# Optimization experiments

Hardware: AMD Instinct MI355X
Metric: run time of the kernel (lower is better)

## Reference

```python
import jax, jax.numpy as jnp
import numpy as np
from jax.scipy.special import logsumexp

B, L, M, D = 8192, 1024, 128, 2  # batch, hilbert.size, bond dim, local_size
MACHINE_POW = 2


def setup_inputs() -> dict:
    key = jax.random.key(0)
    k1, k2 = jax.random.split(key)
    # configurations in the zero-magnetization sector: each row is a permutation
    # of L//2 zeros and L//2 ones (constrained HomogeneousHilbert)
    base = jnp.tile(jnp.arange(D, dtype=jnp.int32), L // D)  # (L,)
    inputs = jax.vmap(lambda k: jax.random.permutation(k, base))(jax.random.split(k1, B))
    # variational parameters epsilon: (local_size, M, size); centered at 1 so the
    # length-L multiplicative cache chain stays in fp32 range
    epsilon = 1.0 + 0.02 * jax.random.normal(k2, (D, M, L), dtype=jnp.float32)
    return {"inputs": inputs, "epsilon": epsilon}


def _conditionals(inputs, epsilon):
    # inputs: (B, L) int in [0, D); epsilon: (D, M, L)
    Bn, Ln = inputs.shape
    Dn, Mn, _ = epsilon.shape
    half = Ln // 2

    def scan_fun(carry, index):
        cache, n_spins = carry                       # (B, D, M), (B, D)
        prev = inputs[:, (index - 1) % Ln]           # (B,) previous-site state
        params_i = epsilon[:, :, index]              # (D, M)
        # irregular gather: cache[b, prev[b], :]
        gathered = jnp.take_along_axis(cache, prev[:, None, None], axis=1)[:, 0, :]  # (B, M)
        prods = params_i[None, :, :] * gathered[:, None, :]  # (B, D, M)
        log_psi = jnp.sum(prods, axis=-1)            # (B, D) sum over bond dim
        n_spins = jnp.where(index > 0,
                            n_spins + jax.nn.one_hot(prev, Dn, dtype=jnp.int32),
                            n_spins)
        # zero-magnetization renormalization: -inf once a local state is exhausted
        renorm = jnp.log(jnp.heaviside((half - n_spins).astype(log_psi.dtype), 0.0))
        return (prods, n_spins), log_psi + renorm

    cache0 = jnp.ones((Bn, Dn, Mn), epsilon.dtype)
    n0 = jnp.zeros((Bn, Dn), jnp.int32)
    _, log_psi = jax.lax.scan(scan_fun, (cache0, n0), jnp.arange(Ln))
    return jnp.transpose(log_psi, (1, 0, 2))  # (B, L, D)


def reference(inputs, epsilon):
    lp = _conditionals(inputs, epsilon)  # (B, L, D)
    # normalize conditionals over local states (machine_pow = 2)
    lp = lp - (1.0 / MACHINE_POW) * logsumexp(MACHINE_POW * lp, axis=-1, keepdims=True)
    # pick the log-conditional of the actual configuration at each site
    sel = jnp.take_along_axis(lp, inputs[:, :, None], axis=2)[:, :, 0]  # (B, L)
    # n_symm = 1 (default apply_symmetries): symmetrized logsumexp is identity
    return jnp.sum(sel, axis=1)  # (B,) log_psi
```

## Files before the change

### kernel.cpp

```cpp
#include <hip/hip_runtime.h>
#include <hip/hip_fp16.h>

typedef unsigned long long u64;
typedef unsigned int uint32;
typedef short short8 __attribute__((ext_vector_type(8)));
typedef float f32x4 __attribute__((ext_vector_type(4)));
typedef _Float16 h2 __attribute__((ext_vector_type(2)));

#define B_N 8192
#define L_N 1024
#define M_N 128
#define C_N 16
#define CH_N 64
#define HALF_N 512

#define OFF_W16  0
#define OFF_R16  0x40000
#define OFF_BITS 0x80000
#define OFF_LR   0x180000
#define OFF_RQ   0x1C0000
#define OFF_T    0x21C0000

#define PACK_BLK 2048
#define PACK_IT  16
#define EPS_BLK  32
#define ZERO_BLK 32

__device__ __forceinline__ unsigned short f32_bf16(float f) {
    union { float f; unsigned u; } x; x.f = f;
    unsigned u = x.u + 0x7FFFu + ((x.u >> 16) & 1u);
    return (unsigned short)(u >> 16);
}

__device__ __forceinline__ float fdot2(h2 a, h2 b, float c) {
#if __has_builtin(__builtin_amdgcn_fdot2)
    return __builtin_amdgcn_fdot2(a, b, c, false);
#else
    return (float)a[0] * (float)b[0] + (float)a[1] * (float)b[1] + c;
#endif
}

__device__ __forceinline__ uint32 fas_u(float f) { union { float f; uint32 u; } x; x.f = f; return x.u; }
__device__ __forceinline__ float uas_f(uint32 u) { union { uint32 u; float f; } x; x.u = u; return x.f; }

template<int CTRL>
__device__ __forceinline__ float dpp_add(float x, float y) {
    union { float f; int i; } a, r;
    a.f = y;
    r.i = __builtin_amdgcn_update_dpp(0, a.i, CTRL, 0xF, 0xF, true);
    return x + r.f;
}

union HU { uint32 u; __half2 hh; h2 v2; };

__global__ __launch_bounds__(256) void k_prep(const int* __restrict__ inp,
        const float* __restrict__ eps, u64* __restrict__ bits,
        _Float16* __restrict__ w16, _Float16* __restrict__ r16,
        unsigned short* __restrict__ lrT, float* __restrict__ out) {
    int bid = blockIdx.x;
    if (bid < PACK_BLK) {
        int g = bid * 256 + threadIdx.x;
        const int stride = PACK_BLK * 256;
        #pragma unroll 4
        for (int it = 0; it < PACK_IT; ++it) {
            int v = inp[g];
            u64 m = __ballot(v != 0);
            if ((threadIdx.x & 63) == 0) bits[g >> 6] = m;
            g += stride;
        }
        return;
    }
    bid -= PACK_BLK;
    if (bid < EPS_BLK) {
        int wid = threadIdx.x >> 6, lane = threadIdx.x & 63;
        int m = bid * 4 + wid;
        const float* e0 = eps + (size_t)m * L_N + lane * 16;
        const float* e1 = eps + (size_t)(M_N + m) * L_N + lane * 16;
        float a[16], b[16];
        #pragma unroll
        for (int j = 0; j < 16; j += 4) {
            *(float4*)&a[j] = *(const float4*)&e0[j];
            *(float4*)&b[j] = *(const float4*)&e1[j];
        }
        float local = 1.f;
        #pragma unroll
        for (int j = 0; j < 16; ++j) local *= a[j];
        float sc = local;
        #pragma unroll
        for (int d = 1; d < 64; d <<= 1) {
            float up = __shfl_up(sc, d);
            if (lane >= d) sc *= up;
        }
        float prev = __shfl_up(sc, 1);
        float E = (lane == 0) ? 1.f : prev;
        int i0 = lane * 16;
        #pragma unroll
        for (int j = 0; j < 16; ++j) {
            float rat = b[j] / a[j];
            w16[(size_t)(i0 + j) * M_N + m] = (_Float16)(E * (a[j] - b[j]));
            r16[(size_t)(i0 + j) * M_N + m] = (_Float16)(rat - 1.f);
            lrT[(size_t)m * L_N + i0 + j] = f32_bf16(__log2f(rat));
            E *= a[j];
        }
        return;
    }
    bid -= EPS_BLK;
    if (bid < ZERO_BLK) {
        out[bid * 256 + threadIdx.x] = 0.f;
    }
}

__global__ __launch_bounds__(256) void k_slog2(const u64* __restrict__ bits,
        const unsigned short* __restrict__ lrT, _Float16* __restrict__ Rq,
        int* __restrict__ T) {
    if (blockIdx.x >= 1024) {
        int b = (blockIdx.x - 1024) * 256 + threadIdx.x;
        const u64* brow = bits + (size_t)b * 16;
        int n1 = 0, n0 = 0, Tv = 1024;
        for (int wd = 0; wd < 16; ++wd) {
            u64 x = brow[wd];
            int pc = __popcll(x);
            if (n1 + pc < HALF_N && n0 + (64 - pc) < HALF_N) {
                n1 += pc; n0 += 64 - pc;
                continue;
            }
            int found = 0;
            for (int k = 0; k < 64; ++k) {
                if (n1 >= HALF_N || n0 >= HALF_N) { Tv = wd * 64 + k; found = 1; break; }
                int sb = (int)((x >> k) & 1);
                n1 += sb; n0 += 1 - sb;
            }
            if (!found) Tv = (wd + 1) * 64;
            break;
        }
        T[b] = Tv;
        return;
    }
    int btile = blockIdx.x >> 1;
    int half = blockIdx.x & 1;
    int wid = threadIdx.x >> 6, lane = threadIdx.x & 63;
    int col = lane & 15, quad = lane >> 4;
    int m = (half * 4 + wid) * 16 + col;
    int b_row = btile * 16 + col;
    const u64* brow = bits + (size_t)b_row * 16;
    const unsigned short* lrow = lrT + (size_t)m * L_N;

    f32x4 cum = (f32x4){0.f, 0.f, 0.f, 0.f};

    for (int c = 0; c < C_N; ++c) {
        #pragma unroll
        for (int reg = 0; reg < 4; ++reg) {
            int b = btile * 16 + quad * 4 + reg;
            Rq[((size_t)c * B_N + b) * M_N + m] = (_Float16)exp2f(cum[reg]);
        }
        u64 wv = brow[c];
        short8 a0, a1;
        #pragma unroll
        for (int j = 0; j < 8; ++j) {
            a0[j] = (short)((((wv >> (quad * 8 + j)) & 1) != 0) ? 0x3F80 : 0);
            a1[j] = (short)((((wv >> (32 + quad * 8 + j)) & 1) != 0) ? 0x3F80 : 0);
        }
        const unsigned short* bp = lrow + c * 64 + quad * 8;
        union { uint4 u; short8 s; } bf0, bf1;
        bf0.u = *(const uint4*)bp;
        bf1.u = *(const uint4*)(bp + 32);
        cum = __builtin_amdgcn_mfma_f32_16x16x32_bf16(a0, bf0.s, cum, 0, 0, 0);
        cum = __builtin_amdgcn_mfma_f32_16x16x32_bf16(a1, bf1.s, cum, 0, 0, 0);
    }
}

__global__ __launch_bounds__(256, 4) void k_main(const u64* __restrict__ bits,
        const _Float16* __restrict__ w16, const _Float16* __restrict__ r16,
        const _Float16* __restrict__ Rq, const int* __restrict__ T,
        float* __restrict__ out) {
    __shared__ _Float16 wbuf[CH_N * M_N];
    __shared__ _Float16 rbuf[CH_N * M_N];
    int c = blockIdx.x & (C_N - 1);
    int bblk = blockIdx.x >> 4;
    int lane = threadIdx.x & 63, wid = threadIdx.x >> 6;
    int s = lane & 15, row = lane >> 4;
    int q = s & 3;
    int b0 = bblk * 64 + wid * 16 + row * 4;

    {
        const uint4* sw = (const uint4*)(w16 + (size_t)c * CH_N * M_N);
        const uint4* sr = (const uint4*)(r16 + (size_t)c * CH_N * M_N);
        uint4* dw = (uint4*)wbuf; uint4* dr = (uint4*)rbuf;
        #pragma unroll
        for (int t = 0; t < 4; ++t) {
            dw[threadIdx.x + t * 256] = sw[threadIdx.x + t * 256];
            dr[threadIdx.x + t * 256] = sr[threadIdx.x + t * 256];
        }
    }

    HU R2[4][4];
    u64 wb[4];
    #pragma unroll
    for (int k = 0; k < 4; ++k) {
        int b = b0 + (q ^ k);
        union { uint4 v; uint32 w[4]; } P;
        P.v = *(const uint4*)(Rq + ((size_t)c * B_N + b) * M_N + s * 8);
        #pragma unroll
        for (int j = 0; j < 4; ++j) R2[k][j].u = P.w[j];
        wb[k] = bits[(size_t)b * 16 + c];
    }
    int Tb = T[b0 + q];

    __syncthreads();

    const float LOG2E2 = 2.885390082f;
    const float NHL2 = -0.3465735903f;
    float sum = 0.f;
    #pragma unroll
    for (int h = 0; h < 2; ++h) {
        uint32 wh[4];
        #pragma unroll
        for (int k = 0; k < 4; ++k) wh[k] = (uint32)(wb[k] >> (h * 32));
        uint32 ows = ~wh[0];
        int rel = Tb - (c * CH_N + h * 32);
        uint32 vmask = (rel <= 0) ? 0u : ((rel >= 32) ? 0xFFFFFFFFu : ((1u << rel) - 1u));

        for (int tt = 0; tt < 32; ++tt) {
            int base = (h * 32 + tt) * M_N + s * 8;
            union { uint4 q4; uint32 w[4]; h2 v2[4]; } W, Rm;
            W.q4 = *(const uint4*)&wbuf[base];
            Rm.q4 = *(const uint4*)&rbuf[base];

            float d[4];
            #pragma unroll
            for (int k = 0; k < 4; ++k) {
                float acc = 0.f;
                #pragma unroll
                for (int j = 0; j < 4; ++j) acc = fdot2(R2[k][j].v2, W.v2[j], acc);
                d[k] = acc;
            }
            float xa = dpp_add<0xB1>(d[0], d[1]);
            float xb = dpp_add<0xB1>(d[2], d[3]);
            float uD = dpp_add<0x4E>(xa, xb);
            uD = dpp_add<0x108>(uD, uD);
            uD = dpp_add<0x104>(uD, uD);

            uint32 sgn = (ows << (31 - tt)) & 0x80000000u;
            float y = uas_f(fas_u(uD) ^ sgn);
            float contr = NHL2 * __log2f(1.f + exp2f(LOG2E2 * y));
            int vm = (int)(vmask << (31 - tt)) >> 31;
            sum += uas_f(fas_u(contr) & (uint32)vm);

            #pragma unroll
            for (int k = 0; k < 4; ++k) {
                uint32 msk = (uint32)((int)(wh[k] << (31 - tt)) >> 31);
                #pragma unroll
                for (int j = 0; j < 4; ++j) {
                    HU sel; sel.u = Rm.w[j] & msk;
                    R2[k][j].v2 += sel.v2 * R2[k][j].v2;
                }
            }
        }
    }
    if (s < 4) atomicAdd(&out[b0 + s], sum);
}

extern "C" void kernel_launch(void* const* d_in, const int* in_sizes, int n_in,
                              void* d_out, int out_size, void* d_ws, size_t ws_size,
                              hipStream_t stream) {
    const int*   inputs  = (const int*)d_in[0];
    const float* epsilon = (const float*)d_in[1];
    float* out = (float*)d_out;

    char* ws = (char*)d_ws;
    _Float16* w16 = (_Float16*)(ws + OFF_W16);
    _Float16* r16 = (_Float16*)(ws + OFF_R16);
    u64*   bits   = (u64*)  (ws + OFF_BITS);
    unsigned short* lrT = (unsigned short*)(ws + OFF_LR);
    _Float16* Rq  = (_Float16*)(ws + OFF_RQ);
    int*   T      = (int*)  (ws + OFF_T);

    k_prep<<<PACK_BLK + EPS_BLK + ZERO_BLK, 256, 0, stream>>>(
        inputs, epsilon, bits, w16, r16, lrT, out);
    k_slog2<<<1024 + 32, 256, 0, stream>>>(bits, lrT, Rq, T);
    k_main<<<(B_N / 64) * C_N, 256, 0, stream>>>(bits, w16, r16, Rq, T, out);
}
```

Baseline: 184.6 us.

## Process 16 bond elements per lane and 128 batches per block in k_main

Each lane of k_main now holds 16 half-precision bond elements per batch row instead of 8, so a group of 8 lanes covers M and each block handles 128 batch rows. The LDS tile of weights is reused across twice as many batches, and one DPP reduction step is dropped. Native exp2/log intrinsics and sbfe bit extracts replace the library calls and shift sequences. In exchange, the doubled register state lowers occupancy (launch bounds go from 4 to 2 blocks) and the grid is half as large.

```diff
diff --git a/kernel.cpp b/kernel.cpp
--- a/kernel.cpp
+++ b/kernel.cpp
@@ -42,6 +42,28 @@
 
 __device__ __forceinline__ uint32 fas_u(float f) { union { float f; uint32 u; } x; x.f = f; return x.u; }
 __device__ __forceinline__ float uas_f(uint32 u) { union { uint32 u; float f; } x; x.u = u; return x.f; }
+
+__device__ __forceinline__ float exp2_n(float x) {
+#if __has_builtin(__builtin_amdgcn_exp2f)
+    return __builtin_amdgcn_exp2f(x);
+#else
+    return exp2f(x);
+#endif
+}
+__device__ __forceinline__ float log2_n(float x) {
+#if __has_builtin(__builtin_amdgcn_logf)
+    return __builtin_amdgcn_logf(x);
+#else
+    return __log2f(x);
+#endif
+}
+__device__ __forceinline__ uint32 bfe1(uint32 v, int off) {
+#if __has_builtin(__builtin_amdgcn_sbfe)
+    return (uint32)__builtin_amdgcn_sbfe((int)v, off, 1);
+#else
+    return (uint32)((int)(v << (31 - off)) >> 31);
+#endif
+}
 
 template<int CTRL>
 __device__ __forceinline__ float dpp_add(float x, float y) {
@@ -151,7 +173,7 @@
         #pragma unroll
         for (int reg = 0; reg < 4; ++reg) {
             int b = btile * 16 + quad * 4 + reg;
-            Rq[((size_t)c * B_N + b) * M_N + m] = (_Float16)exp2f(cum[reg]);
+            Rq[((size_t)c * B_N + b) * M_N + m] = (_Float16)exp2_n(cum[reg]);
         }
         u64 wv = brow[c];
         short8 a0, a1;
@@ -169,7 +191,7 @@
     }
 }
 
-__global__ __launch_bounds__(256, 4) void k_main(const u64* __restrict__ bits,
+__global__ __launch_bounds__(256, 2) void k_main(const u64* __restrict__ bits,
         const _Float16* __restrict__ w16, const _Float16* __restrict__ r16,
         const _Float16* __restrict__ Rq, const int* __restrict__ T,
         float* __restrict__ out) {
@@ -178,9 +200,9 @@
     int c = blockIdx.x & (C_N - 1);
     int bblk = blockIdx.x >> 4;
     int lane = threadIdx.x & 63, wid = threadIdx.x >> 6;
-    int s = lane & 15, row = lane >> 4;
+    int s = lane & 7, grp = lane >> 3;
     int q = s & 3;
-    int b0 = bblk * 64 + wid * 16 + row * 4;
+    int b0 = bblk * 128 + wid * 32 + grp * 4;
 
     {
         const uint4* sw = (const uint4*)(w16 + (size_t)c * CH_N * M_N);
@@ -193,15 +215,16 @@
         }
     }
 
-    HU R2[4][4];
+    HU R2[4][8];
     u64 wb[4];
     #pragma unroll
     for (int k = 0; k < 4; ++k) {
         int b = b0 + (q ^ k);
-        union { uint4 v; uint32 w[4]; } P;
-        P.v = *(const uint4*)(Rq + ((size_t)c * B_N + b) * M_N + s * 8);
-        #pragma unroll
-        for (int j = 0; j < 4; ++j) R2[k][j].u = P.w[j];
+        union { uint4 v[2]; uint32 w[8]; } P;
+        const uint4* src = (const uint4*)(Rq + ((size_t)c * B_N + b) * M_N + s * 16);
+        P.v[0] = src[0]; P.v[1] = src[1];
+        #pragma unroll
+        for (int j = 0; j < 8; ++j) R2[k][j].u = P.w[j];
         wb[k] = bits[(size_t)b * 16 + c];
     }
     int Tb = T[b0 + q];
@@ -221,36 +244,36 @@
         uint32 vmask = (rel <= 0) ? 0u : ((rel >= 32) ? 0xFFFFFFFFu : ((1u << rel) - 1u));
 
         for (int tt = 0; tt < 32; ++tt) {
-            int base = (h * 32 + tt) * M_N + s * 8;
-            union { uint4 q4; uint32 w[4]; h2 v2[4]; } W, Rm;
-            W.q4 = *(const uint4*)&wbuf[base];
-            Rm.q4 = *(const uint4*)&rbuf[base];
+            int base = (h * 32 + tt) * M_N + s * 16;
+            union { uint4 q4[2]; uint32 w[8]; h2 v2[8]; } W, Rm;
+            W.q4[0] = *(const uint4*)&wbuf[base];
+            W.q4[1] = *((const uint4*)&wbuf[base] + 1);
+            Rm.q4[0] = *(const uint4*)&rbuf[base];
+            Rm.q4[1] = *((const uint4*)&rbuf[base] + 1);
 
             float d[4];
             #pragma unroll
             for (int k = 0; k < 4; ++k) {
                 float acc = 0.f;
                 #pragma unroll
-                for (int j = 0; j < 4; ++j) acc = fdot2(R2[k][j].v2, W.v2[j], acc);
+                for (int j = 0; j < 8; ++j) acc = fdot2(R2[k][j].v2, W.v2[j], acc);
                 d[k] = acc;
             }
             float xa = dpp_add<0xB1>(d[0], d[1]);
             float xb = dpp_add<0xB1>(d[2], d[3]);
             float uD = dpp_add<0x4E>(xa, xb);
-            uD = dpp_add<0x108>(uD, uD);
             uD = dpp_add<0x104>(uD, uD);
 
-            uint32 sgn = (ows << (31 - tt)) & 0x80000000u;
+            uint32 sgn = bfe1(ows, tt) & 0x80000000u;
             float y = uas_f(fas_u(uD) ^ sgn);
-            float contr = NHL2 * __log2f(1.f + exp2f(LOG2E2 * y));
-            int vm = (int)(vmask << (31 - tt)) >> 31;
-            sum += uas_f(fas_u(contr) & (uint32)vm);
+            float contr = NHL2 * log2_n(1.f + exp2_n(LOG2E2 * y));
+            sum += uas_f(fas_u(contr) & bfe1(vmask, tt));
 
             #pragma unroll
             for (int k = 0; k < 4; ++k) {
-                uint32 msk = (uint32)((int)(wh[k] << (31 - tt)) >> 31);
+                uint32 msk = bfe1(wh[k], tt);
                 #pragma unroll
-                for (int j = 0; j < 4; ++j) {
+                for (int j = 0; j < 8; ++j) {
                     HU sel; sel.u = Rm.w[j] & msk;
                     R2[k][j].v2 += sel.v2 * R2[k][j].v2;
                 }
@@ -278,5 +301,5 @@
     k_prep<<<PACK_BLK + EPS_BLK + ZERO_BLK, 256, 0, stream>>>(
         inputs, epsilon, bits, w16, r16, lrT, out);
     k_slog2<<<1024 + 32, 256, 0, stream>>>(bits, lrT, Rq, T);
-    k_main<<<(B_N / 64) * C_N, 256, 0, stream>>>(bits, w16, r16, Rq, T, out);
-}
+    k_main<<<(B_N / 128) * C_N, 256, 0, stream>>>(bits, w16, r16, Rq, T, out);
+}
```

Result: faster. 171.3 us (-7.2%).
